# Kernel tuning notes

Measured on AMD Instinct MI355X. Metric: run time of the kernel, lower is better.

Reference implementation:

```python
import jax, jax.numpy as jnp
import numpy as np

WS = 8        # window_size
NH = 16       # num_heads
EPS = 1e-5    # BatchNorm eps (inference mode: running_mean=0, running_var=1)

def conv2d(x, w, padding=0, groups=1):
    return jax.lax.conv_general_dilated(
        x, w, (1, 1), [(padding, padding), (padding, padding)],
        dimension_numbers=('NCHW', 'OIHW', 'NCHW'), feature_group_count=groups)

def bn(x, gamma, beta):
    # eval-mode BatchNorm with running_mean=0, running_var=1
    return x * (gamma / jnp.sqrt(1.0 + EPS))[None, :, None, None] + beta[None, :, None, None]

def avgpool(x, kh, kw, ph, pw):
    # torch AvgPool2d with count_include_pad=True: sum over zero-padded window / (kh*kw)
    s = jax.lax.reduce_window(x, 0.0, jax.lax.add, (1, 1, kh, kw), (1, 1, 1, 1),
                              [(0, 0), (0, 0), (ph, ph), (pw, pw)])
    return s / float(kh * kw)

def rel_pos_index(ws):
    coords = np.stack(np.meshgrid(np.arange(ws), np.arange(ws), indexing='ij')).reshape(2, -1)
    rel = (coords[:, :, None] - coords[:, None, :]).transpose(1, 2, 0) + (ws - 1)
    return (rel[..., 0] * (2 * ws - 1) + rel[..., 1]).reshape(-1)

def hge_kernels(W):
    # build 4 directional Sobel kernels + Gaussian-Laplacian from learned scalars
    S0, S45, S90 = W[:, :, 0, 0], W[:, :, 0, 1], W[:, :, 0, 2]
    S135, GL = W[:, :, 1, 0], W[:, :, 2, 2]
    z = jnp.zeros_like(S0)
    k3 = lambda rows: jnp.stack([jnp.stack(r, -1) for r in rows], -2)  # [O,I,3,3]
    w0 = k3([[S0, 2*S0, S0], [z, z, z], [-S0, -2*S0, -S0]])
    w45 = k3([[2*S45, S45, z], [S45, z, -S45], [z, -S45, -2*S45]])
    w90 = k3([[S90, z, -S90], [2*S90, z, -2*S90], [S90, z, -S90]])
    w135 = k3([[z, -S135, -2*S135], [S135, z, -S135], [2*S135, S135, z]])
    a1 = GL * 4.0; a2 = -a1 / 8.0; a3 = -a1 / 16.0
    wGL = jnp.zeros(S0.shape + (5, 5), S0.dtype)
    for i, j, v in [(0,2,a3),(1,1,a3),(1,2,a2),(1,3,a3),(2,0,a3),(2,1,a2),(2,2,a1),
                    (2,3,a2),(2,4,a3),(3,1,a3),(3,2,a2),(3,3,a3),(4,2,a3)]:
        wGL = wGL.at[:, :, i, j].set(v)
    return w0, w45, w90, w135, wGL

def forward(x, ca_h1, ca_w1, ca_fh, ca_fw, l1_w, l1_g, l1_b, l2_w, l2_g, l2_b,
            hge_w, hge_fc_w, hge_fc_b, qkv_w, rel_table, proj_dw, proj_g, proj_b, proj_pw):
    B, C, H, W = x.shape
    d = C // NH
    scale = d ** -0.5
    # --- CA block: coordinate attention (1x1 convs on H- and W-pooled features) ---
    cm = lambda w, t: jnp.einsum('oc,bc...->bo...', w, t)
    s_h = jax.nn.sigmoid(cm(ca_fh, cm(ca_h1, x.mean(3))))   # [B,C,H]
    s_w = jax.nn.sigmoid(cm(ca_fw, cm(ca_w1, x.mean(2))))   # [B,C,W]
    x = x * s_h[:, :, :, None] * s_w[:, :, None, :]
    # --- local branch: 1x1 ConvBN + 3x3 ConvBN + HGE edge operator ---
    local = bn(conv2d(x, l2_w), l2_g, l2_b) + bn(conv2d(x, l1_w, padding=1), l1_g, l1_b)
    w0, w45, w90, w135, wGL = hge_kernels(hge_w)
    feats = jnp.concatenate([conv2d(x, w0, 1), conv2d(x, w45, 1), conv2d(x, w90, 1),
                             conv2d(x, w135, 1), conv2d(x, wGL, 2)], axis=1)  # [B,5C,H,W]
    local = local + conv2d(feats, hge_fc_w) + hge_fc_b[None, :, None, None]
    # --- windowed attention ---
    ph, pw = (-H) % WS, (-W) % WS
    if ph or pw:
        x = jnp.pad(x, ((0, 0), (0, 0), (0, ph), (0, pw)), mode='reflect')
    Hp, Wp = x.shape[2], x.shape[3]
    hh, ww = Hp // WS, Wp // WS
    qkv = conv2d(x, qkv_w)                                   # [B,3C,Hp,Wp]
    qkv = qkv.reshape(B, 3, NH, d, hh, WS, ww, WS)
    qkv = qkv.transpose(1, 0, 4, 6, 2, 5, 7, 3).reshape(3, B * hh * ww, NH, WS * WS, d)
    q, k, v = qkv[0], qkv[1], qkv[2]
    bias = rel_table[rel_pos_index(WS)].reshape(WS * WS, WS * WS, NH).transpose(2, 0, 1)
    dots = jnp.einsum('wnid,wnjd->wnij', q, k) * scale + bias[None]
    attn = jax.nn.softmax(dots, axis=-1)
    o = jnp.einsum('wnij,wnjd->wnid', attn, v)
    o = o.reshape(B, hh, ww, NH, WS, WS, d).transpose(0, 3, 6, 1, 4, 2, 5)
    o = o.reshape(B, C, Hp, Wp)[:, :, :H, :W]
    # --- directional average pooling of attention output ---
    ox = avgpool(jnp.pad(o, ((0, 0), (0, 0), (0, 1), (0, 0)), mode='reflect'), WS, 1, WS // 2 - 1, 0)
    oy = avgpool(jnp.pad(o, ((0, 0), (0, 0), (0, 0), (0, 1)), mode='reflect'), 1, WS, 0, WS // 2 - 1)
    out = ox + oy + local
    # --- pad_out + separable ConvBN projection (depthwise k=ws -> BN -> 1x1) ---
    out = jnp.pad(out, ((0, 0), (0, 0), (0, 1), (0, 1)), mode='reflect')
    out = conv2d(out, proj_dw, padding=(WS - 1) // 2, groups=C)
    out = bn(out, proj_g, proj_b)
    out = conv2d(out, proj_pw)
    return out[:, :, :H, :W]

def setup_inputs() -> dict:
    key = jax.random.key(0)
    ks = jax.random.split(key, 20)
    C = 128
    f32 = jnp.float32
    n = lambda k, sh, s: jax.random.normal(k, sh, f32) * s
    return {
        'x': jax.random.normal(ks[0], (2, C, 256, 256), f32),
        'ca_h1': n(ks[1], (C, C), 0.05), 'ca_w1': n(ks[2], (C, C), 0.05),
        'ca_fh': n(ks[3], (C, C), 0.05), 'ca_fw': n(ks[4], (C, C), 0.05),
        'l1_w': n(ks[5], (C, C, 3, 3), 0.03),
        'l1_g': 1.0 + n(ks[6], (C,), 0.02), 'l1_b': n(ks[7], (C,), 0.02),
        'l2_w': n(ks[8], (C, C, 1, 1), 0.09),
        'l2_g': 1.0 + n(ks[9], (C,), 0.02), 'l2_b': n(ks[10], (C,), 0.02),
        'hge_w': n(ks[11], (C, C, 3, 3), 0.02),
        'hge_fc_w': n(ks[12], (C, 5 * C, 1, 1), 0.02), 'hge_fc_b': n(ks[13], (C,), 0.02),
        'qkv_w': n(ks[14], (3 * C, C, 1, 1), 0.05),
        'rel_table': n(ks[15], ((2 * WS - 1) ** 2, NH), 0.02),
        'proj_dw': n(ks[16], (C, 1, WS, WS), 0.05),
        'proj_g': 1.0 + n(ks[17], (C,), 0.02), 'proj_b': n(ks[18], (C,), 0.02),
        'proj_pw': n(ks[19], (C, C, 1, 1), 0.05),
    }

def reference(x, ca_h1, ca_w1, ca_fh, ca_fw, l1_w, l1_g, l1_b, l2_w, l2_g, l2_b,
              hge_w, hge_fc_w, hge_fc_b, qkv_w, rel_table, proj_dw, proj_g, proj_b, proj_pw):
    return forward(x, ca_h1, ca_w1, ca_fh, ca_fw, l1_w, l1_g, l1_b, l2_w, l2_g, l2_b,
                   hge_w, hge_fc_w, hge_fc_b, qkv_w, rel_table, proj_dw, proj_g, proj_b, proj_pw)
```

## Files before the change

kernel.cpp:

```cpp
#include <hip/hip_runtime.h>

#define BB 2
#define CC 128
#define HWSZ 65536
#define RSQE 0.9999950000374997f
#define ATT_SCALE 0.35355339059327373f

typedef unsigned short u16;
using short8 = __attribute__((ext_vector_type(8))) short;
using f32x4  = __attribute__((ext_vector_type(4))) float;

#if defined(__has_builtin)
# if __has_builtin(__builtin_amdgcn_fdot2_f32_bf16)
#  define HAVE_DOT2 1
# endif
#endif

__device__ __forceinline__ float b2f(u16 u){
  return __uint_as_float(((unsigned int)u) << 16);
}
__device__ __forceinline__ u16 f2b(float f){
  unsigned int v = __float_as_uint(f);
  unsigned int r = (v + 0x7FFFu + ((v >> 16) & 1u)) >> 16;
  return (u16)r;
}

__global__ void k_detect(const u16* __restrict__ xr, int* __restrict__ flag){
  __shared__ int ws_[4];
  int tid = threadIdx.x;
  int cnt = 0;
  for (int i = 0; i < 16; ++i){
    u16 u = xr[tid*16 + i];
    int e = (u >> 7) & 0xFF;
    cnt += (e < 100 || e > 141) ? 1 : 0;
  }
  #pragma unroll
  for (int off = 32; off > 0; off >>= 1) cnt += __shfl_down(cnt, off, 64);
  if ((tid & 63) == 0) ws_[tid >> 6] = cnt;
  __syncthreads();
  if (tid == 0) *flag = (ws_[0]+ws_[1]+ws_[2]+ws_[3] > 64) ? 1 : 0;
}

__global__ void k_ingest4(const void* __restrict__ src, u16* __restrict__ dst,
                          int n4, const int* __restrict__ flag){
  int i = blockIdx.x * 256 + threadIdx.x;
  if (i >= n4) return;
  if (*flag){
    float4 f = ((const float4*)src)[i];
    ushort4 r; r.x=f2b(f.x); r.y=f2b(f.y); r.z=f2b(f.z); r.w=f2b(f.w);
    ((ushort4*)dst)[i] = r;
  } else {
    ((ushort4*)dst)[i] = ((const ushort4*)src)[i];
  }
}

struct PtrL { const void* p[19]; };

__global__ void k_ingest_w(PtrL pl, u16* __restrict__ dst, const int* __restrict__ flag){
  const int ends[19] = {16384,32768,49152,65536,212992,213120,213248,229632,229760,
                        229888,377344,459264,459392,508544,512144,520336,520464,520592,536976};
  int g = blockIdx.x * 256 + threadIdx.x;
  int idx = g * 4;
  if (idx >= 536976) return;
  int seg = 0, start = 0;
  #pragma unroll
  for (int s = 0; s < 19; ++s){ if (idx >= ends[s]){ seg = s+1; start = ends[s]; } }
  int local = idx - start;
  const void* sp = pl.p[seg];
  if (*flag){
    float4 f = ((const float4*)sp)[local >> 2];
    ushort4 r; r.x=f2b(f.x); r.y=f2b(f.y); r.z=f2b(f.z); r.w=f2b(f.w);
    *(ushort4*)(dst + idx) = r;
  } else {
    *(ushort4*)(dst + idx) = ((const ushort4*)sp)[local >> 2];
  }
}

__global__ void k_prep_A(const u16* __restrict__ fh, const u16* __restrict__ h1,
                         const u16* __restrict__ fw, const u16* __restrict__ w1,
                         const u16* __restrict__ l1b, const u16* __restrict__ l2b,
                         const u16* __restrict__ fcb,
                         float* __restrict__ A_h, float* __restrict__ A_w,
                         float* __restrict__ biasK){
  int idx = blockIdx.x * 256 + threadIdx.x;
  int o = idx >> 7, c = idx & 127;
  float ah = 0.f, aw = 0.f;
  for (int m = 0; m < 128; ++m){
    ah += b2f(fh[o*128 + m]) * b2f(h1[m*128 + c]);
    aw += b2f(fw[o*128 + m]) * b2f(w1[m*128 + c]);
  }
  A_h[idx] = ah; A_w[idx] = aw;
  if (c == 0) biasK[o] = b2f(l1b[o]) + b2f(l2b[o]) + b2f(fcb[o]);
}

__global__ void k_prep_rel(const u16* __restrict__ rel, float* __restrict__ relo){
  int idx = blockIdx.x * 256 + threadIdx.x;
  if (idx >= 3600) return;
  int head = idx / 225, i = idx - head*225;
  relo[idx] = b2f(rel[i*16 + head]);
}

__global__ void k_prep_K(const u16* __restrict__ hge_w, const u16* __restrict__ fc_w,
                         const u16* __restrict__ l1_w, const u16* __restrict__ l1_g,
                         const u16* __restrict__ l2_w, const u16* __restrict__ l2_g,
                         u16* __restrict__ Kwb){
  int idx = blockIdx.x * 256 + threadIdx.x;
  int o = idx >> 7, c = idx & 127;
  float m0=0.f, m45=0.f, m90=0.f, m135=0.f, mgl=0.f;
  const u16* fo = fc_w + o*640;
  for (int m = 0; m < 128; ++m){
    const u16* hw9 = hge_w + (size_t)(m*128 + c)*9;
    m0   += b2f(fo[m      ]) * b2f(hw9[0]);
    m45  += b2f(fo[128 + m]) * b2f(hw9[1]);
    m90  += b2f(fo[256 + m]) * b2f(hw9[2]);
    m135 += b2f(fo[384 + m]) * b2f(hw9[3]);
    mgl  += b2f(fo[512 + m]) * b2f(hw9[8]);
  }
  float g1 = b2f(l1_g[o]) * RSQE;
  float g2 = b2f(l2_g[o]) * RSQE;
  float l1v[9];
  #pragma unroll
  for (int t = 0; t < 9; ++t) l1v[t] = b2f(l1_w[(size_t)idx*9 + t]) * g1;
  float l2v = b2f(l2_w[idx]) * g2;
  float kp[13];
  kp[0]  = -0.25f*mgl;
  kp[1]  =  m0 + 2.f*m45 + m90              - 0.25f*mgl + l1v[0];
  kp[2]  =  2.f*m0 + m45 - m135             - 0.50f*mgl + l1v[1];
  kp[3]  =  m0 - m90 - 2.f*m135             - 0.25f*mgl + l1v[2];
  kp[4]  = -0.25f*mgl;
  kp[5]  =  m45 + 2.f*m90 + m135            - 0.50f*mgl + l1v[3];
  kp[6]  =  4.f*mgl + l1v[4] + l2v;
  kp[7]  = -m45 - 2.f*m90 - m135            - 0.50f*mgl + l1v[5];
  kp[8]  = -0.25f*mgl;
  kp[9]  = -m0 + m90 + 2.f*m135             - 0.25f*mgl + l1v[6];
  kp[10] = -2.f*m0 - m45 + m135             - 0.50f*mgl + l1v[7];
  kp[11] = -m0 - 2.f*m45 - m90              - 0.25f*mgl + l1v[8];
  kp[12] = -0.25f*mgl;
  #pragma unroll
  for (int t = 0; t < 13; ++t) Kwb[t*16384 + idx] = f2b(kp[t]);
}

__global__ void k_means(const u16* __restrict__ x, float* __restrict__ mh, float* __restrict__ mw){
  __shared__ float colpart[4][256];
  int c = blockIdx.x, b = blockIdx.y;
  const u16* xp = x + (size_t)(b*CC + c)*HWSZ;
  int tid = threadIdx.x, lane = tid & 63, wv = tid >> 6;
  float c0=0.f,c1=0.f,c2=0.f,c3=0.f;
  for (int r = 0; r < 64; ++r){
    int h = wv*64 + r;
    ushort4 u = *(const ushort4*)(xp + h*256 + lane*4);
    float v0=b2f(u.x), v1=b2f(u.y), v2=b2f(u.z), v3=b2f(u.w);
    c0+=v0; c1+=v1; c2+=v2; c3+=v3;
    float rs = v0+v1+v2+v3;
    #pragma unroll
    for (int off = 32; off > 0; off >>= 1) rs += __shfl_down(rs, off, 64);
    if (lane == 0) mh[(size_t)(b*CC + c)*256 + h] = rs * (1.0f/256.0f);
  }
  colpart[wv][lane*4+0]=c0; colpart[wv][lane*4+1]=c1;
  colpart[wv][lane*4+2]=c2; colpart[wv][lane*4+3]=c3;
  __syncthreads();
  mw[(size_t)(b*CC + c)*256 + tid] =
    (colpart[0][tid]+colpart[1][tid]+colpart[2][tid]+colpart[3][tid]) * (1.0f/256.0f);
}

__global__ void k_sig(const float* __restrict__ A_h, const float* __restrict__ A_w,
                      const float* __restrict__ mh, const float* __restrict__ mw,
                      float* __restrict__ s_h, float* __restrict__ s_w){
  int o = blockIdx.x, b = blockIdx.y, sel = blockIdx.z, t = threadIdx.x;
  const float* A = sel ? A_w : A_h;
  const float* m = sel ? mw : mh;
  float* s = sel ? s_w : s_h;
  float acc = 0.f;
  for (int c = 0; c < 128; ++c)
    acc += A[o*128 + c] * m[(size_t)(b*CC + c)*256 + t];
  s[(size_t)(b*CC + o)*256 + t] = 1.0f / (1.0f + __expf(-acc));
}

__global__ void k_scale2cl(const u16* __restrict__ cx, const float* __restrict__ s_h,
                           const float* __restrict__ s_w, u16* __restrict__ xcl){
  __shared__ u16 t[16][136];
  int b = blockIdx.z >> 8, h = blockIdx.z & 255;
  int w0 = blockIdx.x * 16;
  int tid = threadIdx.x;
  int ic = tid >> 1, wseg = (tid & 1) * 8;
  uint4 v = *(const uint4*)(cx + (size_t)(b*CC + ic)*HWSZ + h*256 + w0 + wseg);
  float sh = s_h[(size_t)(b*CC + ic)*256 + h];
  const float* swp = s_w + (size_t)(b*CC + ic)*256 + w0 + wseg;
  float4 swa = *(const float4*)swp;
  float4 swb = *(const float4*)(swp + 4);
  u16 tmp[8]; *(uint4*)tmp = v;
  t[wseg+0][ic] = f2b(b2f(tmp[0])*sh*swa.x);
  t[wseg+1][ic] = f2b(b2f(tmp[1])*sh*swa.y);
  t[wseg+2][ic] = f2b(b2f(tmp[2])*sh*swa.z);
  t[wseg+3][ic] = f2b(b2f(tmp[3])*sh*swa.w);
  t[wseg+4][ic] = f2b(b2f(tmp[4])*sh*swb.x);
  t[wseg+5][ic] = f2b(b2f(tmp[5])*sh*swb.y);
  t[wseg+6][ic] = f2b(b2f(tmp[6])*sh*swb.z);
  t[wseg+7][ic] = f2b(b2f(tmp[7])*sh*swb.w);
  __syncthreads();
  int w = tid >> 4, part = (tid & 15) * 8;
  uint4 o = *(const uint4*)&t[w][part];
  *(uint4*)(xcl + ((size_t)(b*256 + h)*256 + (w0 + w))*128 + part) = o;
}

__global__ void k_cf2cl(const u16* __restrict__ src, u16* __restrict__ dst){
  __shared__ u16 t[16][136];
  int b = blockIdx.z >> 8, h = blockIdx.z & 255;
  int w0 = blockIdx.x * 16;
  int tid = threadIdx.x;
  int ic = tid >> 1, wseg = (tid & 1) * 8;
  uint4 v = *(const uint4*)(src + (size_t)(b*CC + ic)*HWSZ + h*256 + w0 + wseg);
  u16 tmp[8]; *(uint4*)tmp = v;
  #pragma unroll
  for (int k = 0; k < 8; ++k) t[wseg + k][ic] = tmp[k];
  __syncthreads();
  int w = tid >> 4, part = (tid & 15) * 8;
  uint4 o = *(const uint4*)&t[w][part];
  *(uint4*)(dst + ((size_t)(b*256 + h)*256 + (w0 + w))*128 + part) = o;
}

__launch_bounds__(256)
__global__ void k_conv5r(const u16* __restrict__ xcl, const u16* __restrict__ Kwb,
                         const float* __restrict__ biasK, u16* __restrict__ outp){
  __shared__ u16 As[132][136];
  int tid = threadIdx.x;
  int wv = tid >> 6, lane = tid & 63;
  int q = lane >> 4, l16 = lane & 15;
  int pt0 = blockIdx.x;
  int pt = (pt0 & 7) * 128 + (pt0 >> 3);
  int b = pt >> 9, h = (pt >> 1) & 255, w0 = (pt & 1) << 7;
  int mrow = (wv & 1) << 6, nrow = (wv >> 1) << 6;
  const u16* xb_b = xcl + (size_t)b*HWSZ*128;
  f32x4 acc[4][4];
  #pragma unroll
  for (int mt = 0; mt < 4; ++mt)
    #pragma unroll
    for (int nt = 0; nt < 4; ++nt) acc[mt][nt] = (f32x4){0.f,0.f,0.f,0.f};

  const int rowTap0[5] = {0,1,4,9,12};
  const int rowNTap[5] = {1,3,5,3,1};
  const int rowDj0[5]  = {0,-1,-2,-1,0};

  for (int ri = 0; ri < 5; ++ri){
    int hh2 = h + ri - 2;
    bool rowok = (unsigned)hh2 < 256u;
    __syncthreads();
    {
      const u16* rowbase = xb_b + (size_t)(rowok ? hh2 : 0)*256*128;
      for (int e = tid; e < 2112; e += 256){
        int px = e >> 4, chunk = (e & 15) << 3;
        int col = w0 - 2 + px;
        uint4 v = {0,0,0,0};
        if (rowok && (unsigned)col < 256u)
          v = *(const uint4*)(rowbase + col*128 + chunk);
        *(uint4*)&As[px][chunk] = v;
      }
    }
    __syncthreads();
    int ntap = rowNTap[ri];
    for (int tt = 0; tt < ntap; ++tt){
      int t = rowTap0[ri] + tt;
      int dj = rowDj0[ri] + tt;
      const u16* Bb = Kwb + t*16384;
      #pragma unroll
      for (int kc = 0; kc < 4; ++kc){
        short8 af[4], bf[4];
        #pragma unroll
        for (int mt = 0; mt < 4; ++mt)
          af[mt] = *(const short8*)&As[mrow + mt*16 + l16 + dj + 2][kc*32 + q*8];
        #pragma unroll
        for (int nt = 0; nt < 4; ++nt)
          bf[nt] = *(const short8*)(Bb + (nrow + nt*16 + l16)*128 + kc*32 + q*8);
        #pragma unroll
        for (int mt = 0; mt < 4; ++mt)
          #pragma unroll
          for (int nt = 0; nt < 4; ++nt)
            acc[mt][nt] = __builtin_amdgcn_mfma_f32_16x16x32_bf16(af[mt], bf[nt], acc[mt][nt], 0, 0, 0);
      }
    }
  }
  #pragma unroll
  for (int nt = 0; nt < 4; ++nt){
    int n = nrow + nt*16 + l16;
    float bv = biasK[n];
    size_t cbase = (size_t)(b*CC + n)*HWSZ + h*256 + w0;
    #pragma unroll
    for (int mt = 0; mt < 4; ++mt){
      int m = mrow + mt*16 + q*4;
      ushort4 st;
      st.x = f2b(acc[mt][nt][0] + bv);
      st.y = f2b(acc[mt][nt][1] + bv);
      st.z = f2b(acc[mt][nt][2] + bv);
      st.w = f2b(acc[mt][nt][3] + bv);
      *(ushort4*)(outp + cbase + m) = st;
    }
  }
}

__launch_bounds__(256)
__global__ void k_mgemm(const u16* __restrict__ Xcl, const u16* __restrict__ W,
                        u16* __restrict__ Y, float* __restrict__ Yf,
                        const int* __restrict__ flag, int nsel, int mode){
  __shared__ u16 As[128][136];
  __shared__ u16 Bs[128][136];
  int tid = threadIdx.x;
  int wv = tid >> 6, lane = tid & 63;
  int q = lane >> 4, l16 = lane & 15;
  int pt = blockIdx.x;
  int b = pt >> 9, h = (pt >> 1) & 255, w0 = (pt & 1) << 7;
  int mrow = (wv & 1) << 6, nrow = (wv >> 1) << 6;
  const u16* Abase = Xcl + ((size_t)(b*256 + h)*256 + w0)*128;
  #pragma unroll
  for (int i = 0; i < 8; ++i){
    int seg = i*256 + tid;
    *(uint4*)&As[seg >> 4][(seg & 15) << 3] = *(const uint4*)(Abase + seg*8);
  }
  for (int sel = 0; sel < nsel; ++sel){
    __syncthreads();
    const u16* Wb = W + sel*16384;
    #pragma unroll
    for (int i = 0; i < 8; ++i){
      int seg = i*256 + tid;
      *(uint4*)&Bs[seg >> 4][(seg & 15) << 3] = *(const uint4*)(Wb + seg*8);
    }
    __syncthreads();
    f32x4 acc[4][4];
    #pragma unroll
    for (int mt = 0; mt < 4; ++mt)
      #pragma unroll
      for (int nt = 0; nt < 4; ++nt) acc[mt][nt] = (f32x4){0.f,0.f,0.f,0.f};
    #pragma unroll
    for (int kc = 0; kc < 4; ++kc){
      short8 af[4], bf[4];
      #pragma unroll
      for (int mt = 0; mt < 4; ++mt) af[mt] = *(const short8*)&As[mrow + mt*16 + l16][kc*32 + q*8];
      #pragma unroll
      for (int nt = 0; nt < 4; ++nt) bf[nt] = *(const short8*)&Bs[nrow + nt*16 + l16][kc*32 + q*8];
      #pragma unroll
      for (int mt = 0; mt < 4; ++mt)
        #pragma unroll
        for (int nt = 0; nt < 4; ++nt)
          acc[mt][nt] = __builtin_amdgcn_mfma_f32_16x16x32_bf16(af[mt], bf[nt], acc[mt][nt], 0, 0, 0);
    }
    if (mode == 0){
      __syncthreads();
      #pragma unroll
      for (int mt = 0; mt < 4; ++mt){
        int m0i = mrow + mt*16 + q*4;
        #pragma unroll
        for (int nt = 0; nt < 4; ++nt){
          int n = nrow + nt*16 + l16;
          Bs[m0i+0][n] = f2b(acc[mt][nt][0]);
          Bs[m0i+1][n] = f2b(acc[mt][nt][1]);
          Bs[m0i+2][n] = f2b(acc[mt][nt][2]);
          Bs[m0i+3][n] = f2b(acc[mt][nt][3]);
        }
      }
      __syncthreads();
      int win = tid >> 4, head = tid & 15;
      size_t obase = (((((size_t)b*32 + (h >> 3))*32 + (w0 >> 3) + win)*3 + sel)*16 + head)*512
                     + (size_t)(h & 7)*64;
      #pragma unroll
      for (int pj = 0; pj < 8; ++pj){
        uint4 vv = *(const uint4*)&Bs[win*8 + pj][head*8];
        *(uint4*)(Y + obase + pj*8) = vv;
      }
    } else {
      int f32o = (Yf != nullptr) && (*flag != 0);
      #pragma unroll
      for (int nt = 0; nt < 4; ++nt){
        int n = nrow + nt*16 + l16;
        size_t cbase = (size_t)(b*CC + n)*HWSZ + h*256 + w0;
        #pragma unroll
        for (int mt = 0; mt < 4; ++mt){
          int m = mrow + mt*16 + q*4;
          if (f32o){
            float4 st; st.x=acc[mt][nt][0]; st.y=acc[mt][nt][1];
            st.z=acc[mt][nt][2]; st.w=acc[mt][nt][3];
            *(float4*)(Yf + cbase + m) = st;
          } else {
            ushort4 st;
            st.x = f2b(acc[mt][nt][0]); st.y = f2b(acc[mt][nt][1]);
            st.z = f2b(acc[mt][nt][2]); st.w = f2b(acc[mt][nt][3]);
            *(ushort4*)(Y + cbase + m) = st;
          }
        }
      }
    }
  }
}

__launch_bounds__(256)
__global__ void k_attn3(const u16* __restrict__ qkvw, const float* __restrict__ relo,
                        u16* __restrict__ obuf){
  __shared__ float relf[228];
  __shared__ u16  kls[4][64][8];
  __shared__ float vls[4][64][8];
  int tid = threadIdx.x, wv = tid >> 6, lane = tid & 63;
  int b = blockIdx.z >> 4, head = blockIdx.z & 15;
  int hh = blockIdx.y, ww = blockIdx.x * 4 + wv;

  for (int e = tid; e < 225; e += 256) relf[e] = relo[head*225 + e];

  size_t base = (((size_t)b*32 + hh)*32 + ww)*3*8192 + (size_t)head*512;
  uint4 qv = *(const uint4*)(qkvw + base + lane*8);
  *(uint4*)&kls[wv][lane][0] = *(const uint4*)(qkvw + base + 8192 + lane*8);
  {
    uint4 raw = *(const uint4*)(qkvw + base + 16384 + lane*8);
    u16 tv[8]; *(uint4*)tv = raw;
    float4 lo, hi;
    lo.x=b2f(tv[0]); lo.y=b2f(tv[1]); lo.z=b2f(tv[2]); lo.w=b2f(tv[3]);
    hi.x=b2f(tv[4]); hi.y=b2f(tv[5]); hi.z=b2f(tv[6]); hi.w=b2f(tv[7]);
    *(float4*)&vls[wv][lane][0] = lo;
    *(float4*)&vls[wv][lane][4] = hi;
  }
  __syncthreads();

  int qi = lane >> 3, qj = lane & 7;
  const float* rbase = relf + (qi + 7)*15 + (qj + 7);
  float s[64];
#if HAVE_DOT2
  typedef __bf16 bf2 __attribute__((ext_vector_type(2)));
  bf2 q0 = __builtin_bit_cast(bf2, qv.x), q1 = __builtin_bit_cast(bf2, qv.y);
  bf2 q2 = __builtin_bit_cast(bf2, qv.z), q3 = __builtin_bit_cast(bf2, qv.w);
  #pragma unroll
  for (int kp = 0; kp < 64; ++kp){
    uint4 kv = *(const uint4*)&kls[wv][kp][0];
    float d = __builtin_amdgcn_fdot2_f32_bf16(q3, __builtin_bit_cast(bf2, kv.w), 0.f, false);
    d = __builtin_amdgcn_fdot2_f32_bf16(q2, __builtin_bit_cast(bf2, kv.z), d, false);
    d = __builtin_amdgcn_fdot2_f32_bf16(q1, __builtin_bit_cast(bf2, kv.y), d, false);
    d = __builtin_amdgcn_fdot2_f32_bf16(q0, __builtin_bit_cast(bf2, kv.x), d, false);
    s[kp] = fmaf(d, ATT_SCALE, rbase[-((kp>>3)*15 + (kp&7))]);
  }
#else
  float qf[8];
  { u16 tq[8]; *(uint4*)tq = qv;
    #pragma unroll
    for (int d = 0; d < 8; ++d) qf[d] = b2f(tq[d]); }
  #pragma unroll
  for (int kp = 0; kp < 64; ++kp){
    uint4 kv = *(const uint4*)&kls[wv][kp][0];
    u16 tk[8]; *(uint4*)tk = kv;
    float d = 0.f;
    #pragma unroll
    for (int dd = 0; dd < 8; ++dd) d = fmaf(qf[dd], b2f(tk[dd]), d);
    s[kp] = fmaf(d, ATT_SCALE, rbase[-((kp>>3)*15 + (kp&7))]);
  }
#endif
  float t16[16];
  #pragma unroll
  for (int i = 0; i < 16; ++i)
    t16[i] = fmaxf(fmaxf(s[i], s[i+16]), fmaxf(s[i+32], s[i+48]));
  float mx = t16[0];
  #pragma unroll
  for (int i = 1; i < 16; ++i) mx = fmaxf(mx, t16[i]);
  #pragma unroll
  for (int kp = 0; kp < 64; ++kp) s[kp] = __expf(s[kp] - mx);
  #pragma unroll
  for (int i = 0; i < 16; ++i)
    t16[i] = (s[i] + s[i+16]) + (s[i+32] + s[i+48]);
  float sum = t16[0];
  #pragma unroll
  for (int i = 1; i < 16; ++i) sum += t16[i];
  float inv = 1.0f / sum;
  float ov[8] = {0.f,0.f,0.f,0.f,0.f,0.f,0.f,0.f};
  #pragma unroll
  for (int kp = 0; kp < 64; ++kp){
    float4 va = *(const float4*)&vls[wv][kp][0];
    float4 vb = *(const float4*)&vls[wv][kp][4];
    float pp = s[kp];
    ov[0] = fmaf(pp, va.x, ov[0]); ov[1] = fmaf(pp, va.y, ov[1]);
    ov[2] = fmaf(pp, va.z, ov[2]); ov[3] = fmaf(pp, va.w, ov[3]);
    ov[4] = fmaf(pp, vb.x, ov[4]); ov[5] = fmaf(pp, vb.y, ov[5]);
    ov[6] = fmaf(pp, vb.z, ov[6]); ov[7] = fmaf(pp, vb.w, ov[7]);
  }
  size_t obase = (size_t)(b*CC + head*8)*HWSZ + (size_t)(hh*8 + qi)*256 + ww*8 + qj;
  #pragma unroll
  for (int d = 0; d < 8; ++d)
    obuf[obase + (size_t)d*HWSZ] = f2b(ov[d] * inv);
}

__launch_bounds__(256)
__global__ void k_pool2(const u16* __restrict__ obuf, u16* __restrict__ localb){
  __shared__ u16 t[71][88];
  int bc = blockIdx.z;
  int h0 = blockIdx.y * 64, w0 = blockIdx.x * 64;
  int tid = threadIdx.x;
  const u16* op = obuf + (size_t)bc * HWSZ;

  for (int e = tid; e < 710; e += 256){
    int tr = e / 10, ci = e - tr*10;
    int gt = h0 - 3 + tr;
    if (gt == 256) gt = 254;
    bool rv = (unsigned)gt <= 255u;
    int g0 = w0 - 8 + ci*8;
    uint4 v = {0,0,0,0};
    if (rv){
      if (g0 >= 0 && g0 <= 248){
        v = *(const uint4*)(op + gt*256 + g0);
      } else {
        u16 tmp[8];
        #pragma unroll
        for (int j = 0; j < 8; ++j){
          int g = g0 + j;
          if (g == 256) g = 254;
          tmp[j] = ((unsigned)g <= 255u) ? op[gt*256 + g] : (u16)0;
        }
        v = *(const uint4*)tmp;
      }
    }
    *(uint4*)&t[tr][ci*8] = v;
  }
  __syncthreads();

  int ty = tid >> 4, tx = tid & 15;
  int r0 = ty*4, c0 = tx*4;
  float sxv[4][4];
  #pragma unroll
  for (int c = 0; c < 4; ++c){
    float col[11];
    #pragma unroll
    for (int i = 0; i < 11; ++i) col[i] = b2f(t[r0+i][c0+8+c]);
    float s = ((col[0]+col[1])+(col[2]+col[3]))+((col[4]+col[5])+(col[6]+col[7]));
    sxv[0][c] = s;
    s += col[8]  - col[0]; sxv[1][c] = s;
    s += col[9]  - col[1]; sxv[2][c] = s;
    s += col[10] - col[2]; sxv[3][c] = s;
  }
  #pragma unroll
  for (int r = 0; r < 4; ++r){
    int rr = r0 + r;
    float pre[11];
    #pragma unroll
    for (int j = 0; j < 11; ++j) pre[j] = b2f(t[rr+3][c0+5+j]);
    float sy0 = ((pre[0]+pre[1])+(pre[2]+pre[3]))+((pre[4]+pre[5])+(pre[6]+pre[7]));
    float sy1 = sy0 + pre[8]  - pre[0];
    float sy2 = sy1 + pre[9]  - pre[1];
    float sy3 = sy2 + pre[10] - pre[2];
    size_t base = (size_t)bc*HWSZ + (size_t)(h0+rr)*256 + (w0+c0);
    ushort4 lv = *(const ushort4*)(localb + base);
    ushort4 st;
    st.x = f2b((sxv[r][0]+sy0)*0.125f + b2f(lv.x));
    st.y = f2b((sxv[r][1]+sy1)*0.125f + b2f(lv.y));
    st.z = f2b((sxv[r][2]+sy2)*0.125f + b2f(lv.z));
    st.w = f2b((sxv[r][3]+sy3)*0.125f + b2f(lv.w));
    *(ushort4*)(localb + base) = st;
  }
}

__launch_bounds__(256)
__global__ void k_dw2(const u16* __restrict__ u_, const u16* __restrict__ dww,
                      const u16* __restrict__ g, const u16* __restrict__ bta,
                      u16* __restrict__ dwout){
  __shared__ u16 xt[71][152];
  int c = blockIdx.z & 127, b = blockIdx.z >> 7;
  int h0 = blockIdx.y * 64, w0 = blockIdx.x * 128;
  int tid = threadIdx.x;
  const u16* up = u_ + (size_t)(b*CC + c)*HWSZ;

  for (int e = tid; e < 71*18; e += 256){
    int tr = e / 18, ci = e - tr*18;
    int gt = h0 - 3 + tr;
    if (gt == 256) gt = 254;
    int g0 = w0 - 8 + ci*8;
    uint4 v = {0,0,0,0};
    if ((unsigned)gt <= 255u){
      if (g0 >= 0 && g0 <= 248){
        v = *(const uint4*)(up + gt*256 + g0);
      } else {
        u16 tmp[8];
        #pragma unroll
        for (int j = 0; j < 8; ++j){
          int gw = g0 + j;
          if (gw == 256) gw = 254;
          tmp[j] = ((unsigned)gw <= 255u) ? up[gt*256 + gw] : (u16)0;
        }
        v = *(const uint4*)tmp;
      }
    }
    *(uint4*)&xt[tr][ci*8] = v;
  }

#if HAVE_DOT2
  typedef __bf16 bf2v __attribute__((ext_vector_type(2)));
  unsigned int wp[32];
  {
    const uint4* wsrc = (const uint4*)(dww + c*64);
    #pragma unroll
    for (int t = 0; t < 8; ++t){
      uint4 v = wsrc[t];
      wp[t*4+0]=v.x; wp[t*4+1]=v.y; wp[t*4+2]=v.z; wp[t*4+3]=v.w;
    }
  }
#else
  float wf[64];
  {
    const u16* wsrc = dww + c*64;
    #pragma unroll
    for (int t = 0; t < 64; ++t) wf[t] = b2f(wsrc[t]);
  }
#endif
  __syncthreads();

  int tx = tid & 15, ty = tid >> 4;
  int r0 = ty*4;
  int cb = tx*8;
  float acc[4][8];
  #pragma unroll
  for (int r = 0; r < 4; ++r)
    #pragma unroll
    for (int k = 0; k < 8; ++k) acc[r][k] = 0.f;

  #pragma unroll
  for (int i = 0; i < 11; ++i){
    const u16* rowp = &xt[r0 + i][cb + 4];
    uint2 av = *(const uint2*)(rowp);
    uint4 mv = *(const uint4*)(rowp + 4);
    uint2 zv = *(const uint2*)(rowp + 12);
    unsigned int d0=av.x, d1=av.y, d2=mv.x, d3=mv.y, d4=mv.z, d5=mv.w, d6=zv.x, d7=zv.y;
    unsigned int dd[8] = {d0,d1,d2,d3,d4,d5,d6,d7};
#if HAVE_DOT2
    unsigned int xp[15];
    #pragma unroll
    for (int t = 1; t < 15; ++t)
      xp[t] = (t & 1) ? ((dd[t>>1] >> 16) | (dd[(t>>1)+1] << 16)) : dd[t>>1];
    #pragma unroll
    for (int dr = 0; dr < 4; ++dr){
      int wr = i - dr;
      if (wr >= 0 && wr < 8){
        #pragma unroll
        for (int k = 0; k < 8; ++k){
          float s = acc[dr][k];
          #pragma unroll
          for (int p = 0; p < 4; ++p)
            s = __builtin_amdgcn_fdot2_f32_bf16(
                  __builtin_bit_cast(bf2v, wp[wr*4+p]),
                  __builtin_bit_cast(bf2v, xp[1+k+2*p]), s, false);
          acc[dr][k] = s;
        }
      }
    }
#else
    float xw[16];
    #pragma unroll
    for (int t = 1; t < 16; ++t){
      unsigned int w32 = dd[t>>1];
      xw[t] = __uint_as_float((t & 1) ? (w32 & 0xFFFF0000u) : (w32 << 16));
    }
    #pragma unroll
    for (int dr = 0; dr < 4; ++dr){
      int wr = i - dr;
      if (wr >= 0 && wr < 8){
        #pragma unroll
        for (int k = 0; k < 8; ++k){
          float s = acc[dr][k];
          #pragma unroll
          for (int j = 0; j < 8; ++j)
            s = fmaf(wf[wr*8+j], xw[1+k+j], s);
          acc[dr][k] = s;
        }
      }
    }
#endif
  }

  float scale = b2f(g[c]) * RSQE;
  float bb = b2f(bta[c]);
  size_t obase = (size_t)(b*CC + c)*HWSZ + (size_t)(h0 + r0)*256 + w0 + cb;
  #pragma unroll
  for (int r = 0; r < 4; ++r){
    u16 po[8];
    #pragma unroll
    for (int k = 0; k < 8; ++k) po[k] = f2b(acc[r][k]*scale + bb);
    *(uint4*)(dwout + obase + (size_t)r*256) = *(uint4*)po;
  }
}

extern "C" void kernel_launch(void* const* d_in, const int* in_sizes, int n_in,
                              void* d_out, int out_size, void* d_ws, size_t ws_size,
                              hipStream_t stream) {
  char* p = (char*)d_ws;
  u16* cx     = (u16*)p; p += 33554432;
  u16* xcl    = (u16*)p; p += 33554432;
  u16* qkvb   = (u16*)p; p += 100663296;
  u16* cw     = (u16*)p; p += 1074176;
  float* A_h    = (float*)p; p += 65536;
  float* A_w    = (float*)p; p += 65536;
  u16*  Kwb     = (u16*)p;  p += 425984;
  float* biasK  = (float*)p; p += 1024;
  float* mh     = (float*)p; p += 262144;
  float* mw     = (float*)p; p += 262144;
  float* s_h    = (float*)p; p += 262144;
  float* s_w    = (float*)p; p += 262144;
  int* flag     = (int*)p;   p += 256;
  float* relo   = (float*)p; p += 16384;

  u16* localb = (u16*)d_out;
  u16* qkvw   = qkvb;
  u16* obuf   = cx;
  u16* dwbuf  = qkvb;
  u16* dwcl   = xcl;

  const int O_h1=0, O_w1=16384, O_fh=32768, O_fw=49152, O_l1w=65536, O_l1g=212992,
            O_l1b=213120, O_l2w=213248, O_l2g=229632, O_l2b=229760, O_hge=229888,
            O_fcw=377344, O_fcb=459264, O_qkvw=459392, O_rel=508544, O_dw=512144,
            O_pg=520336, O_pb=520464, O_pw=520592;

  k_detect<<<1, 256, 0, stream>>>((const u16*)d_in[0], flag);
  k_ingest4<<<16384, 256, 0, stream>>>(d_in[0], cx, 4194304, flag);
  PtrL pl;
  for (int i = 0; i < 19; ++i) pl.p[i] = d_in[i+1];
  k_ingest_w<<<525, 256, 0, stream>>>(pl, cw, flag);

  k_prep_A<<<64, 256, 0, stream>>>(cw+O_fh, cw+O_h1, cw+O_fw, cw+O_w1,
                                   cw+O_l1b, cw+O_l2b, cw+O_fcb, A_h, A_w, biasK);
  k_prep_rel<<<15, 256, 0, stream>>>(cw+O_rel, relo);
  k_prep_K<<<64, 256, 0, stream>>>(cw+O_hge, cw+O_fcw, cw+O_l1w, cw+O_l1g,
                                   cw+O_l2w, cw+O_l2g, Kwb);
  k_means<<<dim3(128, 2), 256, 0, stream>>>(cx, mh, mw);
  k_sig<<<dim3(128, 2, 2), 256, 0, stream>>>(A_h, A_w, mh, mw, s_h, s_w);
  k_scale2cl<<<dim3(16, 1, 512), 256, 0, stream>>>(cx, s_h, s_w, xcl);

  k_conv5r<<<1024, 256, 0, stream>>>(xcl, Kwb, biasK, localb);
  k_mgemm<<<1024, 256, 0, stream>>>(xcl, cw+O_qkvw, qkvw, nullptr, flag, 3, 0);
  k_attn3<<<dim3(8, 32, 32), 256, 0, stream>>>(qkvw, relo, obuf);
  k_pool2<<<dim3(4, 4, 256), 256, 0, stream>>>(obuf, localb);
  k_dw2<<<dim3(2, 4, 256), 256, 0, stream>>>(localb, cw+O_dw, cw+O_pg, cw+O_pb, dwbuf);
  k_cf2cl<<<dim3(16, 1, 512), 256, 0, stream>>>(dwbuf, dwcl);
  k_mgemm<<<1024, 256, 0, stream>>>(dwcl, cw+O_pw, (u16*)d_out, (float*)d_out, flag, 1, 1);
}
```

Baseline: 599.1 us.

## Stage per-tap weights in LDS and reload shifted input rows per tap

The 13-tap conv kernel now loops over taps rather than rows. For each tap it reloads a 128-pixel shifted input row into shared memory and also stages that tap's 128x128 weight tile in shared memory, so the MFMA B operands come from LDS instead of scattered global reads. This removes the strided global weight loads from the inner loop. In exchange it adds 13 input-row loads instead of 5 and 13 barrier pairs instead of 5, and doubles LDS use, which may lower occupancy.

```diff
diff --git a/kernel.cpp b/kernel.cpp
--- a/kernel.cpp
+++ b/kernel.cpp
@@ -24,6 +24,9 @@
   unsigned int r = (v + 0x7FFFu + ((v >> 16) & 1u)) >> 16;
   return (u16)r;
 }
+
+__device__ const int c_DI[13] = {-2,-1,-1,-1, 0, 0,0,0,0, 1,1,1, 2};
+__device__ const int c_DJ[13] = { 0,-1, 0, 1,-2,-1,0,1,2,-1,0,1, 0};
 
 __global__ void k_detect(const u16* __restrict__ xr, int* __restrict__ flag){
   __shared__ int ws_[4];
@@ -220,9 +223,10 @@
 }
 
 __launch_bounds__(256)
-__global__ void k_conv5r(const u16* __restrict__ xcl, const u16* __restrict__ Kwb,
+__global__ void k_conv5t(const u16* __restrict__ xcl, const u16* __restrict__ Kwb,
                          const float* __restrict__ biasK, u16* __restrict__ outp){
-  __shared__ u16 As[132][136];
+  __shared__ u16 As[128][136];
+  __shared__ u16 Bs[128][136];
   int tid = threadIdx.x;
   int wv = tid >> 6, lane = tid & 63;
   int q = lane >> 4, l16 = lane & 15;
@@ -237,46 +241,37 @@
     #pragma unroll
     for (int nt = 0; nt < 4; ++nt) acc[mt][nt] = (f32x4){0.f,0.f,0.f,0.f};
 
-  const int rowTap0[5] = {0,1,4,9,12};
-  const int rowNTap[5] = {1,3,5,3,1};
-  const int rowDj0[5]  = {0,-1,-2,-1,0};
-
-  for (int ri = 0; ri < 5; ++ri){
-    int hh2 = h + ri - 2;
+  for (int t = 0; t < 13; ++t){
+    int di = c_DI[t], dj = c_DJ[t];
+    int hh2 = h + di;
     bool rowok = (unsigned)hh2 < 256u;
+    const u16* rowbase = xb_b + (size_t)(rowok ? hh2 : 0)*256*128;
+    const u16* Bb = Kwb + t*16384;
     __syncthreads();
-    {
-      const u16* rowbase = xb_b + (size_t)(rowok ? hh2 : 0)*256*128;
-      for (int e = tid; e < 2112; e += 256){
-        int px = e >> 4, chunk = (e & 15) << 3;
-        int col = w0 - 2 + px;
-        uint4 v = {0,0,0,0};
-        if (rowok && (unsigned)col < 256u)
-          v = *(const uint4*)(rowbase + col*128 + chunk);
-        *(uint4*)&As[px][chunk] = v;
-      }
+    #pragma unroll
+    for (int i = 0; i < 8; ++i){
+      int seg = i*256 + tid;
+      int px = seg >> 4, chunk = (seg & 15) << 3;
+      int col = w0 + dj + px;
+      uint4 v = {0,0,0,0};
+      if (rowok && (unsigned)col < 256u)
+        v = *(const uint4*)(rowbase + col*128 + chunk);
+      *(uint4*)&As[px][chunk] = v;
+      *(uint4*)&Bs[px][chunk] = *(const uint4*)(Bb + seg*8);
     }
     __syncthreads();
-    int ntap = rowNTap[ri];
-    for (int tt = 0; tt < ntap; ++tt){
-      int t = rowTap0[ri] + tt;
-      int dj = rowDj0[ri] + tt;
-      const u16* Bb = Kwb + t*16384;
-      #pragma unroll
-      for (int kc = 0; kc < 4; ++kc){
-        short8 af[4], bf[4];
-        #pragma unroll
-        for (int mt = 0; mt < 4; ++mt)
-          af[mt] = *(const short8*)&As[mrow + mt*16 + l16 + dj + 2][kc*32 + q*8];
+    #pragma unroll
+    for (int kc = 0; kc < 4; ++kc){
+      short8 af[4], bf[4];
+      #pragma unroll
+      for (int mt = 0; mt < 4; ++mt) af[mt] = *(const short8*)&As[mrow + mt*16 + l16][kc*32 + q*8];
+      #pragma unroll
+      for (int nt = 0; nt < 4; ++nt) bf[nt] = *(const short8*)&Bs[nrow + nt*16 + l16][kc*32 + q*8];
+      #pragma unroll
+      for (int mt = 0; mt < 4; ++mt)
         #pragma unroll
         for (int nt = 0; nt < 4; ++nt)
-          bf[nt] = *(const short8*)(Bb + (nrow + nt*16 + l16)*128 + kc*32 + q*8);
-        #pragma unroll
-        for (int mt = 0; mt < 4; ++mt)
-          #pragma unroll
-          for (int nt = 0; nt < 4; ++nt)
-            acc[mt][nt] = __builtin_amdgcn_mfma_f32_16x16x32_bf16(af[mt], bf[nt], acc[mt][nt], 0, 0, 0);
-      }
+          acc[mt][nt] = __builtin_amdgcn_mfma_f32_16x16x32_bf16(af[mt], bf[nt], acc[mt][nt], 0, 0, 0);
     }
   }
   #pragma unroll
@@ -721,7 +716,7 @@
   k_sig<<<dim3(128, 2, 2), 256, 0, stream>>>(A_h, A_w, mh, mw, s_h, s_w);
   k_scale2cl<<<dim3(16, 1, 512), 256, 0, stream>>>(cx, s_h, s_w, xcl);
 
-  k_conv5r<<<1024, 256, 0, stream>>>(xcl, Kwb, biasK, localb);
+  k_conv5t<<<1024, 256, 0, stream>>>(xcl, Kwb, biasK, localb);
   k_mgemm<<<1024, 256, 0, stream>>>(xcl, cw+O_qkvw, qkvw, nullptr, flag, 3, 0);
   k_attn3<<<dim3(8, 32, 32), 256, 0, stream>>>(qkvw, relo, obuf);
   k_pool2<<<dim3(4, 4, 256), 256, 0, stream>>>(obuf, localb);
```

New measurement: 571.8 us. -4.6%, faster.
